# Kernel optimization log

Measured on AMD Instinct MI355X. Metric: run time of the kernel, lower is better.

## Reference

```python
import jax, jax.numpy as jnp
import numpy as np

N = 50000
E = 800000
IN_C = 128
HID = 64
HEADS = 4
OUT_C = 64


def setup_inputs() -> dict:
    key = jax.random.key(0)
    ks = jax.random.split(key, 20)
    s = 0.05
    inp = {
        "x": jax.random.normal(ks[0], (N, IN_C), dtype=jnp.float32),
        "edge_index": jax.random.randint(ks[1], (2, E), 0, N, dtype=jnp.int64),
        # layer 0: in=128 -> heads=4, C=64
        "W0": jax.random.normal(ks[2], (IN_C, HEADS * HID), jnp.float32) * s,
        "a0s": jax.random.normal(ks[3], (HEADS, HID), jnp.float32) * s,
        "a0d": jax.random.normal(ks[4], (HEADS, HID), jnp.float32) * s,
        "b0": jnp.zeros((HEADS * HID,), jnp.float32),
        # layer 1: 256 -> heads=4, C=64
        "W1": jax.random.normal(ks[5], (HEADS * HID, HEADS * HID), jnp.float32) * s,
        "a1s": jax.random.normal(ks[6], (HEADS, HID), jnp.float32) * s,
        "a1d": jax.random.normal(ks[7], (HEADS, HID), jnp.float32) * s,
        "b1": jnp.zeros((HEADS * HID,), jnp.float32),
        # layer 2: 256 -> heads=1, C=64
        "W2": jax.random.normal(ks[8], (HEADS * HID, HID), jnp.float32) * s,
        "a2s": jax.random.normal(ks[9], (1, HID), jnp.float32) * s,
        "a2d": jax.random.normal(ks[10], (1, HID), jnp.float32) * s,
        "b2": jnp.zeros((HID,), jnp.float32),
        # prediction head: Linear(64 -> 64)
        "hw": jax.random.normal(ks[11], (HID, OUT_C), jnp.float32) * s,
        "hb": jnp.zeros((OUT_C,), jnp.float32),
    }
    return inp


def gat_conv(x, src, dst, W, a_s, a_d, b, heads, n_nodes):
    # x: [N, F_in]; returns [N, heads*C]
    C = a_s.shape[1]
    h = (x @ W).reshape(n_nodes, heads, C)          # [N,H,C]
    alpha_s = jnp.sum(h * a_s, axis=-1)             # [N,H]
    alpha_d = jnp.sum(h * a_d, axis=-1)             # [N,H]
    e = jax.nn.leaky_relu(alpha_s[src] + alpha_d[dst], negative_slope=0.2)  # [E,H]
    m = jax.ops.segment_max(e, dst, num_segments=n_nodes)                  # per-dst max
    ex = jnp.exp(e - m[dst])
    denom = jax.ops.segment_sum(ex, dst, num_segments=n_nodes)
    alpha = ex / (denom[dst] + 1e-16)               # [E,H]
    out = jax.ops.segment_sum(alpha[:, :, None] * h[src], dst, num_segments=n_nodes)
    return out.reshape(n_nodes, heads * C) + b


def reference(x, edge_index, W0, a0s, a0d, b0, W1, a1s, a1d, b1, W2, a2s, a2d, b2, hw, hb):
    n = x.shape[0]
    # PyG GATConv default add_self_loops=True
    loop = jnp.arange(n, dtype=edge_index.dtype)
    src = jnp.concatenate([edge_index[0], loop])
    dst = jnp.concatenate([edge_index[1], loop])

    h = gat_conv(x, src, dst, W0, a0s, a0d, b0, HEADS, n)
    h = jax.nn.relu(h)
    h = gat_conv(h, src, dst, W1, a1s, a1d, b1, HEADS, n)
    h = jax.nn.relu(h)
    h = gat_conv(h, src, dst, W2, a2s, a2d, b2, 1, n)
    # batch is None -> mean over all nodes, keepdim
    g = jnp.mean(h, axis=0, keepdims=True)          # [1, HID]
    return g @ hw + hb                               # [1, OUT_C]
```

## Files before the change

kernel.cpp:

```cpp
#include <hip/hip_runtime.h>
#include <hip/hip_bf16.h>
#include <cstddef>

#define NN 50000
#define EE 800000
#define NB ((NN + 255) / 256)

typedef __attribute__((ext_vector_type(8))) short short8;
typedef __attribute__((ext_vector_type(4))) float f32x4;

__device__ __forceinline__ float leaky(float x) { return x >= 0.f ? x : 0.2f * x; }
__device__ __forceinline__ float bf2f(unsigned short u) {
  return __uint_as_float(((unsigned int)u) << 16);
}
__device__ __forceinline__ float bflo(unsigned int v) { return __uint_as_float(v << 16); }
__device__ __forceinline__ float bfhi(unsigned int v) { return __uint_as_float(v & 0xFFFF0000u); }
__device__ __forceinline__ unsigned short f2bf(float f) {
  __hip_bfloat16 b = __float2bfloat16(f);
  return __builtin_bit_cast(unsigned short, b);
}
__device__ __forceinline__ void accum8(float a, uint4 v, float* acc) {
  acc[0] += a * bflo(v.x); acc[1] += a * bfhi(v.x);
  acc[2] += a * bflo(v.y); acc[3] += a * bfhi(v.y);
  acc[4] += a * bflo(v.z); acc[5] += a * bfhi(v.z);
  acc[6] += a * bflo(v.w); acc[7] += a * bfhi(v.w);
}

__global__ __launch_bounds__(256) void gemm_bf16_k(const unsigned short* __restrict__ A,
                                                   const unsigned short* __restrict__ Bt,
                                                   unsigned short* __restrict__ Cb,
                                                   int K, int Nfull,
                                                   const float* __restrict__ a_s,
                                                   const float* __restrict__ a_d,
                                                   float* __restrict__ als,
                                                   float* __restrict__ ald,
                                                   float* __restrict__ selfex) {
  __shared__ __align__(16) unsigned short As[128 * 40];
  __shared__ __align__(16) unsigned short Bs[64 * 40];
  const int tid = threadIdx.x;
  const int lane = tid & 63;
  const int w = tid >> 6;
  const int bm = blockIdx.x * 128;
  const int bn = blockIdx.y * 64;
  const int quad = lane >> 4;
  const int l16 = lane & 15;
  f32x4 acc[2][4] = {};
  for (int kc = 0; kc < K; kc += 32) {
    {
      int row = tid >> 2, seg = tid & 3;
      int sr = bm + row; if (sr >= NN) sr = NN - 1;
      *(uint4*)&As[row * 40 + seg * 8] = *(const uint4*)(A + (size_t)sr * K + kc + seg * 8);
      row = (tid + 256) >> 2; seg = (tid + 256) & 3;
      sr = bm + row; if (sr >= NN) sr = NN - 1;
      *(uint4*)&As[row * 40 + seg * 8] = *(const uint4*)(A + (size_t)sr * K + kc + seg * 8);
      int n = tid >> 2; seg = tid & 3;
      *(uint4*)&Bs[n * 40 + seg * 8] = *(const uint4*)(Bt + (size_t)(bn + n) * K + kc + seg * 8);
    }
    __syncthreads();
    short8 afr0 = *(const short8*)&As[(w * 32 + l16) * 40 + quad * 8];
    short8 afr1 = *(const short8*)&As[(w * 32 + 16 + l16) * 40 + quad * 8];
#pragma unroll
    for (int nt = 0; nt < 4; ++nt) {
      short8 bfr = *(const short8*)&Bs[(nt * 16 + l16) * 40 + quad * 8];
      acc[0][nt] = __builtin_amdgcn_mfma_f32_16x16x32_bf16(afr0, bfr, acc[0][nt], 0, 0, 0);
      acc[1][nt] = __builtin_amdgcn_mfma_f32_16x16x32_bf16(afr1, bfr, acc[1][nt], 0, 0, 0);
    }
    __syncthreads();
  }
  const int head = bn >> 6;
  const int Hmul = Nfull >> 6;
  float vs[2][4] = {};
  float vd[2][4] = {};
#pragma unroll
  for (int nt = 0; nt < 4; ++nt) {
    const float asv = a_s[head * 64 + nt * 16 + l16];
    const float adv = a_d[head * 64 + nt * 16 + l16];
#pragma unroll
    for (int mt = 0; mt < 2; ++mt)
#pragma unroll
      for (int reg = 0; reg < 4; ++reg) {
        unsigned short c = f2bf(acc[mt][nt][reg]);
        int r = bm + w * 32 + mt * 16 + quad * 4 + reg;
        if (r < NN) Cb[(size_t)r * Nfull + bn + nt * 16 + l16] = c;
        float hv = bf2f(c);
        vs[mt][reg] += hv * asv;
        vd[mt][reg] += hv * adv;
      }
  }
#pragma unroll
  for (int off = 1; off < 16; off <<= 1) {
#pragma unroll
    for (int mt = 0; mt < 2; ++mt)
#pragma unroll
      for (int reg = 0; reg < 4; ++reg) {
        vs[mt][reg] += __shfl_xor(vs[mt][reg], off, 64);
        vd[mt][reg] += __shfl_xor(vd[mt][reg], off, 64);
      }
  }
  if (l16 == 0) {
#pragma unroll
    for (int mt = 0; mt < 2; ++mt)
#pragma unroll
      for (int reg = 0; reg < 4; ++reg) {
        int r = bm + w * 32 + mt * 16 + quad * 4 + reg;
        if (r < NN) {
          als[(size_t)r * Hmul + head] = vs[mt][reg];
          ald[(size_t)r * Hmul + head] = vd[mt][reg];
          selfex[(size_t)r * Hmul + head] = __expf(leaky(vs[mt][reg] + vd[mt][reg]));
        }
      }
  }
}

__global__ __launch_bounds__(256) void hist_k(const int* __restrict__ ei, int* deg) {
  int i = blockIdx.x * 256 + threadIdx.x;
  if (i < EE) atomicAdd(&deg[ei[EE + i]], 1);
}

__global__ __launch_bounds__(256) void scan1_k(const int* __restrict__ deg,
                                               int* __restrict__ incl,
                                               int* __restrict__ partial) {
  __shared__ int s[256];
  int t = threadIdx.x;
  int i = blockIdx.x * 256 + t;
  int v = (i < NN) ? deg[i] : 0;
  s[t] = v;
  __syncthreads();
  for (int off = 1; off < 256; off <<= 1) {
    int u = (t >= off) ? s[t - off] : 0;
    __syncthreads();
    s[t] += u;
    __syncthreads();
  }
  if (i < NN) incl[i] = s[t];
  if (t == 255) partial[blockIdx.x] = s[255];
}

__global__ void scan2_k(int* __restrict__ partial) {
  __shared__ int s[256];
  int t = threadIdx.x;
  int v = (t < NB) ? partial[t] : 0;
  s[t] = v;
  __syncthreads();
  for (int off = 1; off < 256; off <<= 1) {
    int u = (t >= off) ? s[t - off] : 0;
    __syncthreads();
    s[t] += u;
    __syncthreads();
  }
  if (t < NB) partial[t] = s[t] - v;
}

__global__ __launch_bounds__(256) void scan3_k(const int* __restrict__ deg,
                                               const int* __restrict__ incl,
                                               const int* __restrict__ partial,
                                               int* __restrict__ rowptr,
                                               int* __restrict__ cursor) {
  int i = blockIdx.x * 256 + threadIdx.x;
  if (i >= NN) return;
  int r = partial[blockIdx.x] + incl[i] - deg[i];
  rowptr[i] = r;
  cursor[i] = r;
}

__global__ __launch_bounds__(256) void scatter_k(const int* __restrict__ ei,
                                                 int* __restrict__ cursor,
                                                 int* __restrict__ csr_src) {
  int i = blockIdx.x * 256 + threadIdx.x;
  if (i >= EE) return;
  int d = ei[EE + i];
  int p = atomicAdd(&cursor[d], 1);
  csr_src[p] = ei[i];
}

__global__ __launch_bounds__(256) void aggr4c_k(const int* __restrict__ rowptr,
                                                const int* __restrict__ deg,
                                                const int* __restrict__ csr_src,
                                                const float* __restrict__ als,
                                                const float* __restrict__ ald,
                                                const float* __restrict__ selfex,
                                                const uint4* __restrict__ hb4,
                                                const float* __restrict__ bias,
                                                uint4* __restrict__ out4) {
  const int dst = blockIdx.x * 4 + (threadIdx.x >> 6);
  const int lane = threadIdx.x & 63;
  const int slot = lane >> 4;
  const int l16 = lane & 15;
  const int head = l16 >> 2;
  const int rs = rowptr[dst];
  const int dg = deg[dst];
  const float aldv = ald[dst * 4 + head];

  float acc[16] = {};
  float dsum = 0.f;
  if (slot == 0) {
    float a = selfex[dst * 4 + head];
    dsum += a;
    uint4 v0 = hb4[(size_t)dst * 32 + l16 * 2];
    uint4 v1 = hb4[(size_t)dst * 32 + l16 * 2 + 1];
    accum8(a, v0, acc);
    accum8(a, v1, acc + 8);
  }
  int j = slot;
  for (; j + 4 < dg; j += 8) {
    int s0 = csr_src[rs + j];
    int s1 = csr_src[rs + j + 4];
    float e0 = als[s0 * 4 + head];
    float e1 = als[s1 * 4 + head];
    uint4 va0 = hb4[(size_t)s0 * 32 + l16 * 2];
    uint4 vb0 = hb4[(size_t)s0 * 32 + l16 * 2 + 1];
    uint4 va1 = hb4[(size_t)s1 * 32 + l16 * 2];
    uint4 vb1 = hb4[(size_t)s1 * 32 + l16 * 2 + 1];
    float a0 = __expf(leaky(e0 + aldv));
    float a1 = __expf(leaky(e1 + aldv));
    dsum += a0 + a1;
    accum8(a0, va0, acc);
    accum8(a0, vb0, acc + 8);
    accum8(a1, va1, acc);
    accum8(a1, vb1, acc + 8);
  }
  for (; j < dg; j += 4) {
    int s0 = csr_src[rs + j];
    float e0 = als[s0 * 4 + head];
    uint4 va0 = hb4[(size_t)s0 * 32 + l16 * 2];
    uint4 vb0 = hb4[(size_t)s0 * 32 + l16 * 2 + 1];
    float a0 = __expf(leaky(e0 + aldv));
    dsum += a0;
    accum8(a0, va0, acc);
    accum8(a0, vb0, acc + 8);
  }
#pragma unroll
  for (int k = 0; k < 16; ++k) {
    acc[k] += __shfl_xor(acc[k], 16, 64);
    acc[k] += __shfl_xor(acc[k], 32, 64);
  }
  dsum += __shfl_xor(dsum, 16, 64);
  dsum += __shfl_xor(dsum, 32, 64);
  if (slot == 0) {
    const float inv = 1.f / (dsum + 1e-16f);
    const float* bz = bias + l16 * 16;
    uint4 o0, o1;
    float c0, c1;
    c0 = fmaxf(acc[0] * inv + bz[0], 0.f);   c1 = fmaxf(acc[1] * inv + bz[1], 0.f);
    o0.x = ((unsigned int)f2bf(c1) << 16) | f2bf(c0);
    c0 = fmaxf(acc[2] * inv + bz[2], 0.f);   c1 = fmaxf(acc[3] * inv + bz[3], 0.f);
    o0.y = ((unsigned int)f2bf(c1) << 16) | f2bf(c0);
    c0 = fmaxf(acc[4] * inv + bz[4], 0.f);   c1 = fmaxf(acc[5] * inv + bz[5], 0.f);
    o0.z = ((unsigned int)f2bf(c1) << 16) | f2bf(c0);
    c0 = fmaxf(acc[6] * inv + bz[6], 0.f);   c1 = fmaxf(acc[7] * inv + bz[7], 0.f);
    o0.w = ((unsigned int)f2bf(c1) << 16) | f2bf(c0);
    c0 = fmaxf(acc[8] * inv + bz[8], 0.f);   c1 = fmaxf(acc[9] * inv + bz[9], 0.f);
    o1.x = ((unsigned int)f2bf(c1) << 16) | f2bf(c0);
    c0 = fmaxf(acc[10] * inv + bz[10], 0.f); c1 = fmaxf(acc[11] * inv + bz[11], 0.f);
    o1.y = ((unsigned int)f2bf(c1) << 16) | f2bf(c0);
    c0 = fmaxf(acc[12] * inv + bz[12], 0.f); c1 = fmaxf(acc[13] * inv + bz[13], 0.f);
    o1.z = ((unsigned int)f2bf(c1) << 16) | f2bf(c0);
    c0 = fmaxf(acc[14] * inv + bz[14], 0.f); c1 = fmaxf(acc[15] * inv + bz[15], 0.f);
    o1.w = ((unsigned int)f2bf(c1) << 16) | f2bf(c0);
    out4[(size_t)dst * 32 + l16 * 2] = o0;
    out4[(size_t)dst * 32 + l16 * 2 + 1] = o1;
  }
}

__global__ __launch_bounds__(256) void aggr1c_k(const int* __restrict__ rowptr,
                                                const int* __restrict__ deg,
                                                const int* __restrict__ csr_src,
                                                const float* __restrict__ als,
                                                const float* __restrict__ ald,
                                                const float* __restrict__ selfex,
                                                const uint4* __restrict__ hb4,
                                                const float* __restrict__ bias,
                                                float* __restrict__ out) {
  const int dst = blockIdx.x * 4 + (threadIdx.x >> 6);
  const int lane = threadIdx.x & 63;
  const int slot = lane >> 3;
  const int c8 = lane & 7;
  const int rs = rowptr[dst];
  const int dg = deg[dst];
  const float aldv = ald[dst];

  float acc[8] = {};
  float dsum = 0.f;
  if (slot == 0) {
    float a = selfex[dst];
    dsum += a;
    uint4 v = hb4[(size_t)dst * 8 + c8];
    accum8(a, v, acc);
  }
  for (int j = slot; j < dg; j += 8) {
    int s = csr_src[rs + j];
    float e = als[s];
    uint4 v = hb4[(size_t)s * 8 + c8];
    float a = __expf(leaky(e + aldv));
    dsum += a;
    accum8(a, v, acc);
  }
#pragma unroll
  for (int k = 0; k < 8; ++k) {
    acc[k] += __shfl_xor(acc[k], 8, 64);
    acc[k] += __shfl_xor(acc[k], 16, 64);
    acc[k] += __shfl_xor(acc[k], 32, 64);
  }
  dsum += __shfl_xor(dsum, 8, 64);
  dsum += __shfl_xor(dsum, 16, 64);
  dsum += __shfl_xor(dsum, 32, 64);
  if (slot == 0) {
    const float inv = 1.f / (dsum + 1e-16f);
    const float4 bz0 = *(const float4*)(bias + c8 * 8);
    const float4 bz1 = *(const float4*)(bias + c8 * 8 + 4);
    float4 o0 = make_float4(acc[0] * inv + bz0.x, acc[1] * inv + bz0.y,
                            acc[2] * inv + bz0.z, acc[3] * inv + bz0.w);
    float4 o1 = make_float4(acc[4] * inv + bz1.x, acc[5] * inv + bz1.y,
                            acc[6] * inv + bz1.z, acc[7] * inv + bz1.w);
    *(float4*)(out + (size_t)dst * 64 + c8 * 8) = o0;
    *(float4*)(out + (size_t)dst * 64 + c8 * 8 + 4) = o1;
  }
}

__global__ __launch_bounds__(256) void prep_k(const float2* __restrict__ x2,
                                              unsigned int* __restrict__ xb_u,
                                              const float* __restrict__ W0,
                                              unsigned short* __restrict__ W0t,
                                              const float* __restrict__ W1,
                                              unsigned short* __restrict__ W1t,
                                              const float* __restrict__ W2,
                                              unsigned short* __restrict__ W2t) {
  int bid = blockIdx.x;
  int tid = threadIdx.x;
  if (bid < 12500) {
    int i = bid * 256 + tid;
    float2 v = x2[i];
    xb_u[i] = ((unsigned int)f2bf(v.y) << 16) | f2bf(v.x);
    return;
  }
  int r = (bid - 12500) * 256 + tid;
  if (r < 32768) {
    int n = r >> 7, k = r & 127;
    W0t[n * 128 + k] = f2bf(W0[k * 256 + n]);
  } else if (r < 98304) {
    int rr = r - 32768;
    int n = rr >> 8, k = rr & 255;
    W1t[n * 256 + k] = f2bf(W1[k * 256 + n]);
  } else {
    int rr = r - 98304;
    int n = rr >> 8, k = rr & 255;
    W2t[n * 256 + k] = f2bf(W2[k * 64 + n]);
  }
}

__global__ __launch_bounds__(256) void colsum_head_k(const float* __restrict__ h2,
                                                     float* __restrict__ g,
                                                     unsigned int* __restrict__ cnt,
                                                     const float* __restrict__ hw,
                                                     const float* __restrict__ hb,
                                                     float* __restrict__ out) {
  __shared__ float s[256];
  __shared__ float sg[64];
  __shared__ unsigned int sdone;
  int tid = threadIdx.x;
  int c = tid & 63, rg = tid >> 6;
  float acc = 0.f;
  for (int n = blockIdx.x * 4 + rg; n < NN; n += gridDim.x * 4)
    acc += h2[n * 64 + c];
  s[tid] = acc;
  __syncthreads();
  if (tid < 64) atomicAdd(&g[c], s[c] + s[64 + c] + s[128 + c] + s[192 + c]);
  __threadfence();
  __syncthreads();
  if (tid == 0) sdone = atomicAdd(cnt, 1);
  __syncthreads();
  if (sdone != gridDim.x - 1) return;
  if (tid < 64) sg[tid] = atomicAdd(&g[tid], 0.f);
  __syncthreads();
  if (tid < 64) {
    const float invN = 1.0f / (float)NN;
    float a2 = hb[tid];
#pragma unroll 8
    for (int cc = 0; cc < 64; ++cc) a2 += sg[cc] * invN * hw[cc * 64 + tid];
    out[tid] = a2;
  }
}

extern "C" void kernel_launch(void* const* d_in, const int* in_sizes, int n_in,
                              void* d_out, int out_size, void* d_ws, size_t ws_size,
                              hipStream_t stream) {
  const float* x   = (const float*)d_in[0];
  const int*   ei  = (const int*)d_in[1];
  const float* W0  = (const float*)d_in[2];
  const float* a0s = (const float*)d_in[3];
  const float* a0d = (const float*)d_in[4];
  const float* b0  = (const float*)d_in[5];
  const float* W1  = (const float*)d_in[6];
  const float* a1s = (const float*)d_in[7];
  const float* a1d = (const float*)d_in[8];
  const float* b1  = (const float*)d_in[9];
  const float* W2  = (const float*)d_in[10];
  const float* a2s = (const float*)d_in[11];
  const float* a2d = (const float*)d_in[12];
  const float* b2  = (const float*)d_in[13];
  const float* hw  = (const float*)d_in[14];
  const float* hb  = (const float*)d_in[15];
  float* out = (float*)d_out;

  char* w = (char*)d_ws;
  unsigned short* xb   = (unsigned short*)w; w += (size_t)NN * 128 * 2;
  unsigned short* bufG = (unsigned short*)w; w += (size_t)NN * 256 * 2;
  unsigned short* bufA = (unsigned short*)w; w += (size_t)NN * 256 * 2;
  float* bufF = (float*)w;                   w += (size_t)NN * 64 * 4;
  unsigned short* W0t = (unsigned short*)w;  w += 256 * 128 * 2;
  unsigned short* W1t = (unsigned short*)w;  w += 256 * 256 * 2;
  unsigned short* W2t = (unsigned short*)w;  w += 64 * 256 * 2;
  float* als  = (float*)w;    w += (size_t)NN * 4 * 4;
  float* ald  = (float*)w;    w += (size_t)NN * 4 * 4;
  float* sfx  = (float*)w;    w += (size_t)NN * 4 * 4;
  int* deg     = (int*)w;     w += (size_t)NN * 4;
  int* rowptr  = (int*)w;     w += (size_t)NN * 4;
  int* cursor  = (int*)w;     w += (size_t)NN * 4;
  int* incl    = (int*)w;     w += (size_t)NN * 4;
  int* partial = (int*)w;     w += 256 * 4;
  int* csr_src = (int*)w;     w += (size_t)EE * 4;
  float* g    = (float*)w;    w += 256;

  hipMemsetAsync(deg, 0, (size_t)NN * 4, stream);
  hist_k<<<(EE + 255) / 256, 256, 0, stream>>>(ei, deg);
  scan1_k<<<NB, 256, 0, stream>>>(deg, incl, partial);
  scan2_k<<<1, 256, 0, stream>>>(partial);
  scan3_k<<<NB, 256, 0, stream>>>(deg, incl, partial, rowptr, cursor);
  scatter_k<<<(EE + 255) / 256, 256, 0, stream>>>(ei, cursor, csr_src);

  prep_k<<<12500 + 448, 256, 0, stream>>>((const float2*)x, (unsigned int*)xb,
                                          W0, W0t, W1, W1t, W2, W2t);

  const int GX = (NN + 127) / 128;
  const int GA = NN / 4;

  auto layer4 = [&](const unsigned short* in, int K, const unsigned short* Wt,
                    const float* a_s, const float* a_d, const float* bias,
                    unsigned short* hbuf, unsigned short* obuf) {
    gemm_bf16_k<<<dim3(GX, 4), 256, 0, stream>>>(in, Wt, hbuf, K, 256,
                                                 a_s, a_d, als, ald, sfx);
    aggr4c_k<<<GA, 256, 0, stream>>>(rowptr, deg, csr_src, als, ald, sfx,
                                     (const uint4*)hbuf, bias, (uint4*)obuf);
  };

  layer4(xb, 128, W0t, a0s, a0d, b0, bufG, bufA);
  layer4(bufA, 256, W1t, a1s, a1d, b1, bufG, bufA);

  gemm_bf16_k<<<dim3(GX, 1), 256, 0, stream>>>(bufA, W2t, bufG, 256, 64,
                                               a2s, a2d, als, ald, sfx);
  aggr1c_k<<<GA, 256, 0, stream>>>(rowptr, deg, csr_src, als, ald, sfx,
                                   (const uint4*)bufG, b2, bufF);

  hipMemsetAsync(g, 0, 68 * 4, stream);
  colsum_head_k<<<256, 256, 0, stream>>>(bufF, g, (unsigned int*)(g + 64), hw, hb, out);
}
```

Baseline: 440.9 us.

## Stage edge indices and attention weights in shared memory per 64-edge chunk

```diff
diff --git a/kernel.cpp b/kernel.cpp
--- a/kernel.cpp
+++ b/kernel.cpp
@@ -18,6 +18,11 @@
 __device__ __forceinline__ unsigned short f2bf(float f) {
   __hip_bfloat16 b = __float2bfloat16(f);
   return __builtin_bit_cast(unsigned short, b);
+}
+__device__ __forceinline__ float selh(float4 v, int h) {
+  float a = (h & 1) ? v.y : v.x;
+  float b = (h & 1) ? v.w : v.z;
+  return (h & 2) ? b : a;
 }
 __device__ __forceinline__ void accum8(float a, uint4 v, float* acc) {
   acc[0] += a * bflo(v.x); acc[1] += a * bfhi(v.x);
@@ -182,14 +187,19 @@
                                                 const uint4* __restrict__ hb4,
                                                 const float* __restrict__ bias,
                                                 uint4* __restrict__ out4) {
-  const int dst = blockIdx.x * 4 + (threadIdx.x >> 6);
+  __shared__ int sidx[4][64];
+  __shared__ float4 salf[4][64];
+  const int wv = threadIdx.x >> 6;
+  const int dst0 = blockIdx.x * 4;
+  const int dst = dst0 + wv;
   const int lane = threadIdx.x & 63;
   const int slot = lane >> 4;
   const int l16 = lane & 15;
   const int head = l16 >> 2;
   const int rs = rowptr[dst];
   const int dg = deg[dst];
-  const float aldv = ald[dst * 4 + head];
+  const int maxdg = max(max(deg[dst0], deg[dst0 + 1]), max(deg[dst0 + 2], deg[dst0 + 3]));
+  const float4 ald4 = *(const float4*)(ald + (size_t)dst * 4);
 
   float acc[16] = {};
   float dsum = 0.f;
@@ -201,33 +211,48 @@
     accum8(a, v0, acc);
     accum8(a, v1, acc + 8);
   }
-  int j = slot;
-  for (; j + 4 < dg; j += 8) {
-    int s0 = csr_src[rs + j];
-    int s1 = csr_src[rs + j + 4];
-    float e0 = als[s0 * 4 + head];
-    float e1 = als[s1 * 4 + head];
-    uint4 va0 = hb4[(size_t)s0 * 32 + l16 * 2];
-    uint4 vb0 = hb4[(size_t)s0 * 32 + l16 * 2 + 1];
-    uint4 va1 = hb4[(size_t)s1 * 32 + l16 * 2];
-    uint4 vb1 = hb4[(size_t)s1 * 32 + l16 * 2 + 1];
-    float a0 = __expf(leaky(e0 + aldv));
-    float a1 = __expf(leaky(e1 + aldv));
-    dsum += a0 + a1;
-    accum8(a0, va0, acc);
-    accum8(a0, vb0, acc + 8);
-    accum8(a1, va1, acc);
-    accum8(a1, vb1, acc + 8);
-  }
-  for (; j < dg; j += 4) {
-    int s0 = csr_src[rs + j];
-    float e0 = als[s0 * 4 + head];
-    uint4 va0 = hb4[(size_t)s0 * 32 + l16 * 2];
-    uint4 vb0 = hb4[(size_t)s0 * 32 + l16 * 2 + 1];
-    float a0 = __expf(leaky(e0 + aldv));
-    dsum += a0;
-    accum8(a0, va0, acc);
-    accum8(a0, vb0, acc + 8);
+
+  for (int chunk = 0; chunk < maxdg; chunk += 64) {
+    int n = dg - chunk;
+    __syncthreads();
+    if (lane < n) {
+      int s = csr_src[rs + chunk + lane];
+      float4 as4 = *(const float4*)(als + (size_t)s * 4);
+      float4 e;
+      e.x = __expf(leaky(as4.x + ald4.x));
+      e.y = __expf(leaky(as4.y + ald4.y));
+      e.z = __expf(leaky(as4.z + ald4.z));
+      e.w = __expf(leaky(as4.w + ald4.w));
+      sidx[wv][lane] = s;
+      salf[wv][lane] = e;
+    }
+    __syncthreads();
+    int m = n < 64 ? n : 64;
+    int j = slot;
+    for (; j + 4 < m; j += 8) {
+      int s0 = sidx[wv][j];
+      int s1 = sidx[wv][j + 4];
+      float a0 = selh(salf[wv][j], head);
+      float a1 = selh(salf[wv][j + 4], head);
+      uint4 va0 = hb4[(size_t)s0 * 32 + l16 * 2];
+      uint4 vb0 = hb4[(size_t)s0 * 32 + l16 * 2 + 1];
+      uint4 va1 = hb4[(size_t)s1 * 32 + l16 * 2];
+      uint4 vb1 = hb4[(size_t)s1 * 32 + l16 * 2 + 1];
+      dsum += a0 + a1;
+      accum8(a0, va0, acc);
+      accum8(a0, vb0, acc + 8);
+      accum8(a1, va1, acc);
+      accum8(a1, vb1, acc + 8);
+    }
+    for (; j < m; j += 4) {
+      int s0 = sidx[wv][j];
+      float a0 = selh(salf[wv][j], head);
+      uint4 va0 = hb4[(size_t)s0 * 32 + l16 * 2];
+      uint4 vb0 = hb4[(size_t)s0 * 32 + l16 * 2 + 1];
+      dsum += a0;
+      accum8(a0, va0, acc);
+      accum8(a0, vb0, acc + 8);
+    }
   }
 #pragma unroll
   for (int k = 0; k < 16; ++k) {
@@ -271,12 +296,17 @@
                                                 const uint4* __restrict__ hb4,
                                                 const float* __restrict__ bias,
                                                 float* __restrict__ out) {
-  const int dst = blockIdx.x * 4 + (threadIdx.x >> 6);
+  __shared__ int sidx[4][64];
+  __shared__ float salf[4][64];
+  const int wv = threadIdx.x >> 6;
+  const int dst0 = blockIdx.x * 4;
+  const int dst = dst0 + wv;
   const int lane = threadIdx.x & 63;
   const int slot = lane >> 3;
   const int c8 = lane & 7;
   const int rs = rowptr[dst];
   const int dg = deg[dst];
+  const int maxdg = max(max(deg[dst0], deg[dst0 + 1]), max(deg[dst0 + 2], deg[dst0 + 3]));
   const float aldv = ald[dst];
 
   float acc[8] = {};
@@ -287,13 +317,35 @@
     uint4 v = hb4[(size_t)dst * 8 + c8];
     accum8(a, v, acc);
   }
-  for (int j = slot; j < dg; j += 8) {
-    int s = csr_src[rs + j];
-    float e = als[s];
-    uint4 v = hb4[(size_t)s * 8 + c8];
-    float a = __expf(leaky(e + aldv));
-    dsum += a;
-    accum8(a, v, acc);
+  for (int chunk = 0; chunk < maxdg; chunk += 64) {
+    int n = dg - chunk;
+    __syncthreads();
+    if (lane < n) {
+      int s = csr_src[rs + chunk + lane];
+      sidx[wv][lane] = s;
+      salf[wv][lane] = __expf(leaky(als[s] + aldv));
+    }
+    __syncthreads();
+    int m = n < 64 ? n : 64;
+    int j = slot;
+    for (; j + 8 < m; j += 16) {
+      int s0 = sidx[wv][j];
+      int s1 = sidx[wv][j + 8];
+      float a0 = salf[wv][j];
+      float a1 = salf[wv][j + 8];
+      uint4 v0 = hb4[(size_t)s0 * 8 + c8];
+      uint4 v1 = hb4[(size_t)s1 * 8 + c8];
+      dsum += a0 + a1;
+      accum8(a0, v0, acc);
+      accum8(a1, v1, acc);
+    }
+    for (; j < m; j += 8) {
+      int s = sidx[wv][j];
+      float a = salf[wv][j];
+      uint4 v = hb4[(size_t)s * 8 + c8];
+      dsum += a;
+      accum8(a, v, acc);
+    }
   }
 #pragma unroll
   for (int k = 0; k < 8; ++k) {
```

Result: no change. 440.1 us (-0.2%).

## Use direct global-to-LDS loads with XOR swizzle in GEMM and fuse scan/memset launches

Applied to the files above, without the earlier changes.

```diff
diff --git a/kernel.cpp b/kernel.cpp
--- a/kernel.cpp
+++ b/kernel.cpp
@@ -8,6 +8,9 @@
 
 typedef __attribute__((ext_vector_type(8))) short short8;
 typedef __attribute__((ext_vector_type(4))) float f32x4;
+
+#define GLB __attribute__((address_space(1)))
+#define LDS __attribute__((address_space(3)))
 
 __device__ __forceinline__ float leaky(float x) { return x >= 0.f ? x : 0.2f * x; }
 __device__ __forceinline__ float bf2f(unsigned short u) {
@@ -18,6 +21,11 @@
 __device__ __forceinline__ unsigned short f2bf(float f) {
   __hip_bfloat16 b = __float2bfloat16(f);
   return __builtin_bit_cast(unsigned short, b);
+}
+__device__ __forceinline__ float selh(float4 v, int h) {
+  float a = (h & 1) ? v.y : v.x;
+  float b = (h & 1) ? v.w : v.z;
+  return (h & 2) ? b : a;
 }
 __device__ __forceinline__ void accum8(float a, uint4 v, float* acc) {
   acc[0] += a * bflo(v.x); acc[1] += a * bfhi(v.x);
@@ -35,8 +43,8 @@
                                                    float* __restrict__ als,
                                                    float* __restrict__ ald,
                                                    float* __restrict__ selfex) {
-  __shared__ __align__(16) unsigned short As[128 * 40];
-  __shared__ __align__(16) unsigned short Bs[64 * 40];
+  __shared__ __align__(16) unsigned short As[128 * 32];
+  __shared__ __align__(16) unsigned short Bs[64 * 32];
   const int tid = threadIdx.x;
   const int lane = tid & 63;
   const int w = tid >> 6;
@@ -44,24 +52,35 @@
   const int bn = blockIdx.y * 64;
   const int quad = lane >> 4;
   const int l16 = lane & 15;
+  const int lrow = lane >> 2;
+  const int lseg = lane & 3;
   f32x4 acc[2][4] = {};
   for (int kc = 0; kc < K; kc += 32) {
+#pragma unroll
+    for (int c = 0; c < 2; ++c) {
+      int row = w * 32 + c * 16 + lrow;
+      int g = lseg ^ ((row >> 2) & 3);
+      int sr = bm + row; if (sr >= NN) sr = NN - 1;
+      const unsigned short* gp = A + (size_t)sr * K + kc + g * 8;
+      __builtin_amdgcn_global_load_lds((const GLB void*)gp,
+                                       (LDS void*)&As[(w * 32 + c * 16) * 32], 16, 0, 0);
+    }
     {
-      int row = tid >> 2, seg = tid & 3;
-      int sr = bm + row; if (sr >= NN) sr = NN - 1;
-      *(uint4*)&As[row * 40 + seg * 8] = *(const uint4*)(A + (size_t)sr * K + kc + seg * 8);
-      row = (tid + 256) >> 2; seg = (tid + 256) & 3;
-      sr = bm + row; if (sr >= NN) sr = NN - 1;
-      *(uint4*)&As[row * 40 + seg * 8] = *(const uint4*)(A + (size_t)sr * K + kc + seg * 8);
-      int n = tid >> 2; seg = tid & 3;
-      *(uint4*)&Bs[n * 40 + seg * 8] = *(const uint4*)(Bt + (size_t)(bn + n) * K + kc + seg * 8);
+      int row = w * 16 + lrow;
+      int g = lseg ^ ((row >> 2) & 3);
+      const unsigned short* gp = Bt + (size_t)(bn + row) * K + kc + g * 8;
+      __builtin_amdgcn_global_load_lds((const GLB void*)gp,
+                                       (LDS void*)&Bs[(w * 16) * 32], 16, 0, 0);
     }
     __syncthreads();
-    short8 afr0 = *(const short8*)&As[(w * 32 + l16) * 40 + quad * 8];
-    short8 afr1 = *(const short8*)&As[(w * 32 + 16 + l16) * 40 + quad * 8];
+    const int ra0 = w * 32 + l16;
+    const int ra1 = ra0 + 16;
+    short8 afr0 = *(const short8*)&As[ra0 * 32 + ((quad ^ ((ra0 >> 2) & 3)) << 3)];
+    short8 afr1 = *(const short8*)&As[ra1 * 32 + ((quad ^ ((ra1 >> 2) & 3)) << 3)];
 #pragma unroll
     for (int nt = 0; nt < 4; ++nt) {
-      short8 bfr = *(const short8*)&Bs[(nt * 16 + l16) * 40 + quad * 8];
+      int rb = nt * 16 + l16;
+      short8 bfr = *(const short8*)&Bs[rb * 32 + ((quad ^ ((rb >> 2) & 3)) << 3)];
       acc[0][nt] = __builtin_amdgcn_mfma_f32_16x16x32_bf16(afr0, bfr, acc[0][nt], 0, 0, 0);
       acc[1][nt] = __builtin_amdgcn_mfma_f32_16x16x32_bf16(afr1, bfr, acc[1][nt], 0, 0, 0);
     }
@@ -136,8 +155,13 @@
   if (t == 255) partial[blockIdx.x] = s[255];
 }
 
-__global__ void scan2_k(int* __restrict__ partial) {
+__global__ __launch_bounds__(256) void scan23_k(const int* __restrict__ deg,
+                                                const int* __restrict__ incl,
+                                                const int* __restrict__ partial,
+                                                int* __restrict__ rowptr,
+                                                int* __restrict__ cursor) {
   __shared__ int s[256];
+  __shared__ int ex[256];
   int t = threadIdx.x;
   int v = (t < NB) ? partial[t] : 0;
   s[t] = v;
@@ -148,19 +172,15 @@
     s[t] += u;
     __syncthreads();
   }
-  if (t < NB) partial[t] = s[t] - v;
-}
-
-__global__ __launch_bounds__(256) void scan3_k(const int* __restrict__ deg,
-                                               const int* __restrict__ incl,
-                                               const int* __restrict__ partial,
-                                               int* __restrict__ rowptr,
-                                               int* __restrict__ cursor) {
-  int i = blockIdx.x * 256 + threadIdx.x;
-  if (i >= NN) return;
-  int r = partial[blockIdx.x] + incl[i] - deg[i];
-  rowptr[i] = r;
-  cursor[i] = r;
+  ex[t] = s[t] - v;
+  __syncthreads();
+  int base = ex[blockIdx.x];
+  int i = blockIdx.x * 256 + t;
+  if (i < NN) {
+    int r = base + incl[i] - deg[i];
+    rowptr[i] = r;
+    cursor[i] = r;
+  }
 }
 
 __global__ __launch_bounds__(256) void scatter_k(const int* __restrict__ ei,
@@ -324,7 +344,9 @@
                                               const float* __restrict__ W1,
                                               unsigned short* __restrict__ W1t,
                                               const float* __restrict__ W2,
-                                              unsigned short* __restrict__ W2t) {
+                                              unsigned short* __restrict__ W2t,
+                                              int* __restrict__ deg,
+                                              float* __restrict__ g) {
   int bid = blockIdx.x;
   int tid = threadIdx.x;
   if (bid < 12500) {
@@ -333,19 +355,28 @@
     xb_u[i] = ((unsigned int)f2bf(v.y) << 16) | f2bf(v.x);
     return;
   }
-  int r = (bid - 12500) * 256 + tid;
-  if (r < 32768) {
-    int n = r >> 7, k = r & 127;
-    W0t[n * 128 + k] = f2bf(W0[k * 256 + n]);
-  } else if (r < 98304) {
-    int rr = r - 32768;
-    int n = rr >> 8, k = rr & 255;
-    W1t[n * 256 + k] = f2bf(W1[k * 256 + n]);
-  } else {
-    int rr = r - 98304;
-    int n = rr >> 8, k = rr & 255;
-    W2t[n * 256 + k] = f2bf(W2[k * 64 + n]);
-  }
+  if (bid < 12948) {
+    int r = (bid - 12500) * 256 + tid;
+    if (r < 32768) {
+      int n = r >> 7, k = r & 127;
+      W0t[n * 128 + k] = f2bf(W0[k * 256 + n]);
+    } else if (r < 98304) {
+      int rr = r - 32768;
+      int n = rr >> 8, k = rr & 255;
+      W1t[n * 256 + k] = f2bf(W1[k * 256 + n]);
+    } else {
+      int rr = r - 98304;
+      int n = rr >> 8, k = rr & 255;
+      W2t[n * 256 + k] = f2bf(W2[k * 64 + n]);
+    }
+    return;
+  }
+  if (bid < 13144) {
+    int i = (bid - 12948) * 256 + tid;
+    if (i < NN) deg[i] = 0;
+    return;
+  }
+  if (tid < 68) g[tid] = 0.f;
 }
 
 __global__ __launch_bounds__(256) void colsum_head_k(const float* __restrict__ h2,
@@ -421,15 +452,13 @@
   int* csr_src = (int*)w;     w += (size_t)EE * 4;
   float* g    = (float*)w;    w += 256;
 
-  hipMemsetAsync(deg, 0, (size_t)NN * 4, stream);
+  prep_k<<<13145, 256, 0, stream>>>((const float2*)x, (unsigned int*)xb,
+                                    W0, W0t, W1, W1t, W2, W2t, deg, g);
+
   hist_k<<<(EE + 255) / 256, 256, 0, stream>>>(ei, deg);
   scan1_k<<<NB, 256, 0, stream>>>(deg, incl, partial);
-  scan2_k<<<1, 256, 0, stream>>>(partial);
-  scan3_k<<<NB, 256, 0, stream>>>(deg, incl, partial, rowptr, cursor);
+  scan23_k<<<NB, 256, 0, stream>>>(deg, incl, partial, rowptr, cursor);
   scatter_k<<<(EE + 255) / 256, 256, 0, stream>>>(ei, cursor, csr_src);
-
-  prep_k<<<12500 + 448, 256, 0, stream>>>((const float2*)x, (unsigned int*)xb,
-                                          W0, W0t, W1, W1t, W2, W2t);
 
   const int GX = (NN + 127) / 128;
   const int GA = NN / 4;
@@ -451,6 +480,5 @@
   aggr1c_k<<<GA, 256, 0, stream>>>(rowptr, deg, csr_src, als, ald, sfx,
                                    (const uint4*)bufG, b2, bufF);
 
-  hipMemsetAsync(g, 0, 68 * 4, stream);
   colsum_head_k<<<256, 256, 0, stream>>>(bufF, g, (unsigned int*)(g + 64), hw, hb, out);
 }
```

New measurement: 437.5 us. About the same (-0.8%).
